# Optimization experiments

Measured on AMD Instinct MI355X. Metric: run time of the kernel, lower is better.

## Reference

```python
import jax, jax.numpy as jnp
import numpy as np

L = 48                 # lattice side
M = 2 * L * L          # 4608 spin-orbitals (spinful: 2 per site)
N_OCC = 1024           # occupied fermions
N_HID = 24             # hidden fermions
NT2 = 2 * N_HID        # pairing channels in CNN output
JASTROW = 16
CH = NT2 + JASTROW     # 64 CNN channels
NBLOCKS = 4
K = 3                  # conv kernel size


def conv2d_circular(x, w, b):
    # x: (C,H,W), w: (O,I,K,K); 'SAME' conv with circular (periodic) padding
    p = K // 2
    xp = jnp.pad(x, ((0, 0), (p, p), (p, p)), mode='wrap')
    y = jax.lax.conv_general_dilated(xp[None], w, (1, 1), 'VALID',
                                     dimension_numbers=('NCHW', 'OIHW', 'NCHW'))[0]
    if b is not None:
        y = y + b[:, None, None]
    return y


def cnn_forward(x, params):
    # ReshapeConv: flat spinful config (M,) -> (2, L, L)
    h = x.reshape(2, L, L)
    for i, (w1, b1, w2, b2) in enumerate(params):
        res = h
        t = h / jnp.sqrt(i + 1.0)
        t = t / jnp.sqrt(2.0) if i == 0 else jax.nn.gelu(t)
        t = jax.nn.gelu(conv2d_circular(t, w1, b1))
        t = conv2d_circular(t, w2, b2)
        if t.shape[0] > res.shape[0]:
            res = jnp.repeat(res, t.shape[0] // res.shape[0], axis=0)
        h = t + res
    return h / jnp.sqrt(NBLOCKS + 1.0)


def pfaffian_sign(A):
    # Sign of the Pfaffian of skew-symmetric A via Householder tridiagonalization.
    # pf(A) = det(Q) * prod(superdiag of T over even positions); det(Q)=(-1)^{#reflections}.
    n = A.shape[0]
    idx = jnp.arange(n)

    def body(k, carry):
        A, ds = carry
        col = A[:, k]
        xv = jnp.where(idx > k, col, 0.0)
        normx = jnp.sqrt(jnp.sum(xv * xv))
        s = jnp.where(col[k + 1] >= 0, 1.0, -1.0)
        v = xv - (-s * normx) * (idx == k + 1).astype(A.dtype)
        vn = jnp.sqrt(jnp.sum(v * v))
        ok = vn > 1e-30
        v = jnp.where(ok, v / jnp.where(ok, vn, 1.0), 0.0)
        u = A @ v
        # H A H for skew A with H = I - 2 v v^T  (v^T A v = 0)
        A = A + 2.0 * jnp.outer(v, u) - 2.0 * jnp.outer(u, v)
        return A, jnp.where(ok, -ds, ds)

    A, ds = jax.lax.fori_loop(0, n - 2, body, (A, jnp.array(1.0, A.dtype)))
    sup = jnp.diagonal(A, offset=1)[::2]
    return ds * jnp.prod(jnp.sign(sup))


def setup_inputs() -> dict:
    key = jax.random.key(0)
    ks = jax.random.split(key, 32)
    # occupation config in {+1,-1} with exactly N_OCC occupied modes
    occ = jnp.concatenate([jnp.ones(N_OCC, jnp.float32), -jnp.ones(M - N_OCC, jnp.float32)])
    x = jax.random.permutation(ks[0], occ)

    def he(k, shape):
        fan_in = shape[1] * shape[2] * shape[3]
        return jax.random.normal(k, shape, jnp.float32) * jnp.sqrt(2.0 / fan_in)

    inp = {
        'x': x,
        'F_vv': jax.random.normal(ks[1], (M, M), jnp.float32),
        'F_hh': jax.random.normal(ks[2], (N_HID, N_HID), jnp.float32),
    }
    j = 3
    for b in range(NBLOCKS):
        cin = 2 if b == 0 else CH
        inp[f'w1_{b}'] = he(ks[j], (CH, cin, K, K)); j += 1
        inp[f'b1_{b}'] = jnp.zeros((CH,), jnp.float32)
        inp[f'w2_{b}'] = he(ks[j], (CH, CH, K, K)); j += 1
        if b < NBLOCKS - 1:  # last block conv2 has no bias
            inp[f'b2_{b}'] = jnp.zeros((CH,), jnp.float32)
    return inp


def reference(x, F_vv, F_hh,
              w1_0, b1_0, w2_0, b2_0,
              w1_1, b1_1, w2_1, b2_1,
              w1_2, b1_2, w2_2, b2_2,
              w1_3, b1_3, w2_3):
    params = [(w1_0, b1_0, w2_0, b2_0),
              (w1_1, b1_1, w2_1, b2_1),
              (w1_2, b1_2, w2_2, b2_2),
              (w1_3, b1_3, w2_3, None)]
    out = cnn_forward(x, params)                     # (CH, L, L)
    n = jnp.nonzero(x == 1, size=N_OCC)[0]           # occupied mode indices
    log_J = out[NT2:].sum()                          # Jastrow log-factor (real)
    F_vh = out[:NT2].reshape(-1, M).T                # (M, N_HID)
    Fvv = 0.5 * (F_vv - F_vv.T)
    Fvh_n = F_vh[n]                                  # (N_OCC, N_HID)
    A = jnp.block([[Fvv[n][:, n], Fvh_n],
                   [-Fvh_n.T, 0.5 * (F_hh - F_hh.T)]])  # (N_OCC+N_HID,)^2 skew
    sign = pfaffian_sign(jax.lax.stop_gradient(A))   # cos(angle(sign)) == sign for real dtype
    logabspf = 0.5 * jnp.linalg.slogdet(A)[1]        # |pf(A)| = sqrt(|det(A)|)
    return sign, logabspf + log_J
```

## Files before the change

kernel.cpp:

```cpp
#include <hip/hip_runtime.h>
#include <math.h>


#define NPIX 2304
#define MSZ  4608
#define NOCC 1024
#define NHID 24
#define PF_N 1048

__device__ __forceinline__ float gelu_f(float v){
  float v3 = v*v*v;
  return 0.5f*v*(1.0f + tanhf(0.7978845608028654f*(v + 0.044715f*v3)));
}

__global__ void k_find_n(const float* __restrict__ x, int* __restrict__ nidx){
  __shared__ int cnt[256];
  __shared__ int off[256];
  int t = threadIdx.x;
  int c = 0;
  for (int k = 0; k < 18; k++) c += (x[t*18+k] == 1.0f) ? 1 : 0;
  cnt[t] = c;
  __syncthreads();
  if (t == 0){ int s = 0; for (int q=0;q<256;q++){ off[q]=s; s+=cnt[q]; } }
  __syncthreads();
  int o = off[t];
  for (int k = 0; k < 18; k++){
    int idx = t*18+k;
    if (x[idx] == 1.0f) nidx[o++] = idx;
  }
}

__global__ void k_pre(const float* __restrict__ in, float* __restrict__ outp,
                      int count, int dogelu, float scale){
  int g = blockIdx.x*256 + threadIdx.x;
  if (g >= count) return;
  float v = in[g]*scale;
  if (dogelu) v = gelu_f(v);
  outp[g] = v;
}

__global__ __launch_bounds__(256) void k_conv(const float* __restrict__ in,
      const float* __restrict__ wgt, const float* __restrict__ bias,
      const float* __restrict__ res, float* __restrict__ outp,
      int cin, int resmode, int dogelu, float scale){
  int c = blockIdx.x / 9;
  int p = (blockIdx.x % 9)*256 + threadIdx.x;
  int y = p / 48, x = p - y*48;
  int ym = ((y+47)%48)*48, y0 = y*48, yp = ((y+1)%48)*48;
  int xm = (x+47)%48, xq = (x+1)%48;
  float s = 0.f;
  const float* wp = wgt + c*cin*9;
  for (int ci = 0; ci < cin; ci++){
    const float* b_ = in + ci*NPIX;
    s += b_[ym+xm]*wp[0] + b_[ym+x]*wp[1] + b_[ym+xq]*wp[2]
       + b_[y0+xm]*wp[3] + b_[y0+x]*wp[4] + b_[y0+xq]*wp[5]
       + b_[yp+xm]*wp[6] + b_[yp+x]*wp[7] + b_[yp+xq]*wp[8];
    wp += 9;
  }
  if (bias) s += bias[c];
  if (dogelu) s = gelu_f(s);
  if (resmode == 1) s += res[c*NPIX + p];
  else if (resmode == 2) s += res[(c>>5)*NPIX + p];
  s *= scale;
  outp[c*NPIX + p] = s;
}

__global__ void k_logJ(const float* __restrict__ hfin, double* __restrict__ acc){
  int g = blockIdx.x*256 + threadIdx.x;
  double v = (double)hfin[48*NPIX + g];
  for (int o = 32; o > 0; o >>= 1) v += __shfl_down(v, o, 64);
  __shared__ double wsum[4];
  int lane = threadIdx.x & 63, wv = threadIdx.x >> 6;
  if (lane == 0) wsum[wv] = v;
  __syncthreads();
  if (threadIdx.x == 0) atomicAdd(acc, wsum[0]+wsum[1]+wsum[2]+wsum[3]);
}

__device__ __forceinline__ double fvh_val(const float* h, int m, int r){
  int s = (m >= NPIX) ? 1 : 0;
  int p = m - s*NPIX;
  return (double)h[(2*r+s)*NPIX + p];
}

__global__ void k_buildA(const float* __restrict__ Fvv, const float* __restrict__ Fhh,
                         const float* __restrict__ hfin, const int* __restrict__ nidx,
                         double* __restrict__ A){
  int g = blockIdx.x*256 + threadIdx.x;
  if (g >= PF_N*PF_N) return;
  int i = g / PF_N, j = g - i*PF_N;
  if (j >= i) return;
  double v;
  if (i < NOCC){
    int ni = nidx[i], nj = nidx[j];
    v = 0.5*((double)Fvv[(size_t)ni*MSZ + nj] - (double)Fvv[(size_t)nj*MSZ + ni]);
  } else if (j < NOCC){
    v = -fvh_val(hfin, nidx[j], i - NOCC);
  } else {
    int r = i - NOCC, r2 = j - NOCC;
    v = 0.5*((double)Fhh[r*NHID + r2] - (double)Fhh[r2*NHID + r]);
  }
  A[(size_t)i*PF_N + j] = v;
}

__device__ __forceinline__ void factor_lds(double* D, double* sTf, int w,
      double* __restrict__ histN, double* __restrict__ lacc,
      int* __restrict__ nneg){
  const int tid = threadIdx.x;
  const int r = tid & 63, qu = tid >> 6;
  const int np = w >> 1;
  for (int j = 0; j < np; j++){
    const int r0 = 2*j, r1 = r0 + 1;
    const double t = -D[r1*65 + r0];
    const double invt = 1.0 / t;
    if (tid == 0) sTf[j] = t;
    const bool rowok = (r < w) && (r >= r0 + 2);
    if (rowok){
      const double ar = D[r*65 + r0], br = D[r*65 + r1];
      if (qu == 0){
        histN[32 + j*64 + r]        = ar * invt;
        histN[32 + 2048 + j*64 + r] = br * invt;
      }
      const int lo = r0 + 2, hi = r;
      const int per = (hi - lo + 3) >> 2;
      const int cb = lo + qu*per;
      int ce = cb + per; if (ce > hi) ce = hi;
      for (int c = cb; c < ce; c++){
        const double ac = D[c*65 + r0], bc = D[c*65 + r1];
        D[r*65 + c] += (br*ac - ar*bc) * invt;
      }
    }
    __syncthreads();
  }
  if (tid < np) histN[tid] = 1.0 / sTf[tid];
  if (tid < 64){
    double lv = 0.0; int sg = 0;
    if (tid < np){ double t = sTf[tid]; lv = log(fabs(t)); sg = (t < 0.0) ? 1 : 0; }
    for (int o = 32; o > 0; o >>= 1){
      lv += __shfl_down(lv, o, 64);
      sg += __shfl_down(sg, o, 64);
    }
    if (tid == 0){ atomicAdd(lacc, lv); atomicAdd(nneg, sg); }
  }
}

__global__ __launch_bounds__(256) void k_panelD0(const double* __restrict__ A,
      double* __restrict__ hist, double* __restrict__ lacc,
      int* __restrict__ nneg){
  __shared__ double D[64*65];
  __shared__ double sTf[32];
  const int tid = threadIdx.x;
  for (int idx = tid; idx < 64*64; idx += 256){
    int r = idx >> 6, c = idx & 63;
    if (r > c) D[r*65+c] = A[(size_t)r*PF_N + c];
  }
  __syncthreads();
  factor_lds(D, sTf, 64, hist, lacc, nneg);
}

__global__ __launch_bounds__(256) void k_panelR(double* __restrict__ A,
      const double* __restrict__ hist, int k){
  const int N = PF_N, c0 = 64*k, tc0 = c0 + 64;
  const int wv = threadIdx.x >> 6, lc = threadIdx.x & 63;
  const int i = tc0 + blockIdx.x*4 + wv;
  if (i >= N) return;
  double v = A[(size_t)i*N + c0 + lc];
  const double* hA = hist + 32;
  const double* hB = hist + 32 + 2048;
  #pragma unroll 8
  for (int j = 0; j < 32; j++){
    double a = __shfl(v, 2*j,   64);
    double b = __shfl(v, 2*j+1, 64);
    if (lc >= 2*j+2) v += b*hA[j*64+lc] - a*hB[j*64+lc];
  }
  A[(size_t)i*N + c0 + lc] = v;
}

__global__ __launch_bounds__(256) void k_trail(double* __restrict__ A,
      const double* __restrict__ histR, double* __restrict__ histW,
      double* __restrict__ lacc, int* __restrict__ nneg, int k){
  const int N = PF_N, c0 = 64*k, tc0 = c0 + 64;
  const int tid = threadIdx.x;
  int I = 0, item = blockIdx.x;
  while ((I+1)*(I+2)/2 <= item) I++;
  const int J = item - I*(I+1)/2;
  const int i0 = tc0 + I*64, j0 = tc0 + J*64;
  const int iend = (i0 + 64 < N) ? (i0 + 64) : N;
  const int jend = (j0 + 64 < N) ? (j0 + 64) : N;
  __shared__ double shmem[4224];
  __shared__ double sInvL[32];
  __shared__ double sTf[32];
  double* sPiA = shmem;
  double* sPiB = shmem + 1056;
  double* sPjA = shmem + 2112;
  double* sPjB = shmem + 3168;
  if (tid < 32) sInvL[tid] = histR[tid];
  const int ty = tid >> 4, tx = tid & 15;
  double acc[4][4];
  #pragma unroll
  for (int rr = 0; rr < 4; rr++)
    #pragma unroll
    for (int cc = 0; cc < 4; cc++){
      const int i = i0 + ty + 16*rr, j = j0 + tx + 16*cc;
      acc[rr][cc] = (i < iend && j < jend && i > j) ? A[(size_t)i*N + j] : 0.0;
    }
  __syncthreads();
  #pragma unroll
  for (int lh = 0; lh < 2; lh++){
    #pragma unroll
    for (int u = 0; u < 4; u++){
      const int idx = tid + u*256;
      const int r = idx >> 4, ll = idx & 15;
      const int l = lh*16 + ll;
      const double it = sInvL[l];
      const int gi = i0 + r;
      double a = 0.0, b = 0.0;
      if (gi < iend){
        a = A[(size_t)gi*N + c0 + 2*l];
        b = A[(size_t)gi*N + c0 + 2*l + 1];
      }
      sPiA[ll*66+r] = a; sPiB[ll*66+r] = b;
      const int gj = j0 + r;
      double a2 = 0.0, b2 = 0.0;
      if (gj < jend){
        a2 = A[(size_t)gj*N + c0 + 2*l];
        b2 = A[(size_t)gj*N + c0 + 2*l + 1];
      }
      sPjA[ll*66+r] = a2*it; sPjB[ll*66+r] = b2*it;
    }
    __syncthreads();
    #pragma unroll 4
    for (int ll = 0; ll < 16; ll++){
      double ar[4], br[4], ac[4], bc[4];
      #pragma unroll
      for (int rr = 0; rr < 4; rr++){
        ar[rr] = sPiA[ll*66 + ty + 16*rr];
        br[rr] = sPiB[ll*66 + ty + 16*rr];
      }
      #pragma unroll
      for (int cc = 0; cc < 4; cc++){
        ac[cc] = sPjA[ll*66 + tx + 16*cc];
        bc[cc] = sPjB[ll*66 + tx + 16*cc];
      }
      #pragma unroll
      for (int rr = 0; rr < 4; rr++)
        #pragma unroll
        for (int cc = 0; cc < 4; cc++)
          acc[rr][cc] += br[rr]*ac[cc] - ar[rr]*bc[cc];
    }
    __syncthreads();
  }
  #pragma unroll
  for (int rr = 0; rr < 4; rr++)
    #pragma unroll
    for (int cc = 0; cc < 4; cc++){
      const int i = i0 + ty + 16*rr, j = j0 + tx + 16*cc;
      if (i < iend && j < jend && i > j) A[(size_t)i*N + j] = acc[rr][cc];
    }
  if (blockIdx.x == 0){
    __syncthreads();
    const int wn = iend - i0;
    #pragma unroll
    for (int rr = 0; rr < 4; rr++)
      #pragma unroll
      for (int cc = 0; cc < 4; cc++){
        const int i = i0 + ty + 16*rr, j = j0 + tx + 16*cc;
        if (i < iend && j < jend && i > j)
          shmem[(i - i0)*65 + (j - j0)] = acc[rr][cc];
      }
    __syncthreads();
    factor_lds(shmem, sTf, wn, histW, lacc, nneg);
  }
}

__global__ void k_out(const double* __restrict__ lacc, const int* __restrict__ nneg,
                      const double* __restrict__ logJ, float* __restrict__ outp){
  if (threadIdx.x == 0){
    outp[0] = (*nneg & 1) ? -1.0f : 1.0f;
    outp[1] = (float)(*lacc + *logJ);
  }
}

extern "C" void kernel_launch(void* const* d_in, const int* in_sizes, int n_in,
                              void* d_out, int out_size, void* d_ws, size_t ws_size,
                              hipStream_t stream){
  (void)in_sizes; (void)n_in; (void)out_size; (void)ws_size;
  const float* x   = (const float*)d_in[0];
  const float* Fvv = (const float*)d_in[1];
  const float* Fhh = (const float*)d_in[2];
  const float* w1[4] = {(const float*)d_in[3], (const float*)d_in[7],
                        (const float*)d_in[11], (const float*)d_in[15]};
  const float* b1[4] = {(const float*)d_in[4], (const float*)d_in[8],
                        (const float*)d_in[12], (const float*)d_in[16]};
  const float* w2[4] = {(const float*)d_in[5], (const float*)d_in[9],
                        (const float*)d_in[13], (const float*)d_in[17]};
  const float* b2[3] = {(const float*)d_in[6], (const float*)d_in[10],
                        (const float*)d_in[14]};

  char* ws = (char*)d_ws;
  double* lacc  = (double*)(ws + 0);
  int*    nneg  = (int*)(ws + 8);
  double* logJa = (double*)(ws + 1024);
  int*    nidx  = (int*)(ws + 1088);
  double* hist0 = (double*)(ws + 8192);
  double* hist1 = (double*)(ws + 41216);
  const size_t CB = 589824;
  float* tbuf  = (float*)(ws + 74240);
  float* ybuf  = (float*)(ws + 74240 + CB);
  float* hbuf0 = (float*)(ws + 74240 + 2*CB);
  float* hbuf1 = (float*)(ws + 74240 + 3*CB);
  double* A    = (double*)(ws + 74240 + 4*CB);

  hipMemsetAsync(d_ws, 0, 2048, stream);
  k_find_n<<<1,256,0,stream>>>(x, nidx);

  k_pre <<<18, 256,0,stream>>>(x, tbuf, 4608, 0, 0.70710678118654752f);
  k_conv<<<576,256,0,stream>>>(tbuf, w1[0], b1[0], nullptr, ybuf, 2, 0, 1, 1.0f);
  k_conv<<<576,256,0,stream>>>(ybuf, w2[0], b2[0], x,      hbuf0, 64, 2, 0, 1.0f);
  k_pre <<<576,256,0,stream>>>(hbuf0, tbuf, 147456, 1, 0.70710678118654752f);
  k_conv<<<576,256,0,stream>>>(tbuf, w1[1], b1[1], nullptr, ybuf, 64, 0, 1, 1.0f);
  k_conv<<<576,256,0,stream>>>(ybuf, w2[1], b2[1], hbuf0,  hbuf1, 64, 1, 0, 1.0f);
  k_pre <<<576,256,0,stream>>>(hbuf1, tbuf, 147456, 1, 0.57735026918962576f);
  k_conv<<<576,256,0,stream>>>(tbuf, w1[2], b1[2], nullptr, ybuf, 64, 0, 1, 1.0f);
  k_conv<<<576,256,0,stream>>>(ybuf, w2[2], b2[2], hbuf1,  hbuf0, 64, 1, 0, 1.0f);
  k_pre <<<576,256,0,stream>>>(hbuf0, tbuf, 147456, 1, 0.5f);
  k_conv<<<576,256,0,stream>>>(tbuf, w1[3], b1[3], nullptr, ybuf, 64, 0, 1, 1.0f);
  k_conv<<<576,256,0,stream>>>(ybuf, w2[3], nullptr, hbuf0, hbuf1, 64, 1, 0,
                               0.44721359549995794f);

  k_logJ  <<<144,256,0,stream>>>(hbuf1, logJa);
  k_buildA<<<(PF_N*PF_N+255)/256,256,0,stream>>>(Fvv, Fhh, hbuf1, nidx, A);

  k_panelD0<<<1,256,0,stream>>>(A, hist0, lacc, nneg);
  for (int k = 0; k < 16; k++){
    double* hR = (k & 1) ? hist1 : hist0;
    double* hW = (k & 1) ? hist0 : hist1;
    const int m = PF_N - 64*(k+1);
    k_panelR<<<(m+3)/4,256,0,stream>>>(A, hR, k);
    const int nt = (m + 63) >> 6;
    k_trail<<<nt*(nt+1)/2,256,0,stream>>>(A, hR, hW, lacc, nneg, k);
  }
  k_out<<<1,64,0,stream>>>(lacc, nneg, logJa, (float*)d_out);
}
```

Baseline: 1.128 ms.

## Fuse CNN pre-activation and logJ into conv, tile Fvv gather, fold output into trail

The pre-activation (scale+gelu) pass is folded into the conv epilogue, and the x scaling is moved into the index-finding kernel. The Jastrow sum is reduced inside the last conv. Each conv thread now computes three horizontally adjacent outputs so neighbouring input loads are reused. The Fvv gather for A is done in 32x32 shared-memory tiles over the lower triangle only, so the transposed read is coalesced. The final output write is moved into the last trailing-update kernel, which removes the separate output launch. This cuts launches and memory traffic at the cost of a more complex conv epilogue, and correctness of the final output now depends on the atomic return values and on that block finishing last.

```diff
diff --git a/kernel.cpp b/kernel.cpp
--- a/kernel.cpp
+++ b/kernel.cpp
@@ -13,12 +13,18 @@
   return 0.5f*v*(1.0f + tanhf(0.7978845608028654f*(v + 0.044715f*v3)));
 }
 
-__global__ void k_find_n(const float* __restrict__ x, int* __restrict__ nidx){
+__global__ void k_prep(const float* __restrict__ x, int* __restrict__ nidx,
+                       float* __restrict__ tbuf){
   __shared__ int cnt[256];
   __shared__ int off[256];
   int t = threadIdx.x;
   int c = 0;
-  for (int k = 0; k < 18; k++) c += (x[t*18+k] == 1.0f) ? 1 : 0;
+  for (int k = 0; k < 18; k++){
+    int idx = t*18 + k;
+    float v = x[idx];
+    c += (v == 1.0f) ? 1 : 0;
+    tbuf[idx] = v * 0.70710678118654752f;
+  }
   cnt[t] = c;
   __syncthreads();
   if (t == 0){ int s = 0; for (int q=0;q<256;q++){ off[q]=s; s+=cnt[q]; } }
@@ -30,81 +36,108 @@
   }
 }
 
-__global__ void k_pre(const float* __restrict__ in, float* __restrict__ outp,
-                      int count, int dogelu, float scale){
-  int g = blockIdx.x*256 + threadIdx.x;
-  if (g >= count) return;
-  float v = in[g]*scale;
-  if (dogelu) v = gelu_f(v);
-  outp[g] = v;
-}
-
-__global__ __launch_bounds__(256) void k_conv(const float* __restrict__ in,
+__global__ __launch_bounds__(128) void k_conv(const float* __restrict__ in,
       const float* __restrict__ wgt, const float* __restrict__ bias,
       const float* __restrict__ res, float* __restrict__ outp,
-      int cin, int resmode, int dogelu, float scale){
-  int c = blockIdx.x / 9;
-  int p = (blockIdx.x % 9)*256 + threadIdx.x;
-  int y = p / 48, x = p - y*48;
-  int ym = ((y+47)%48)*48, y0 = y*48, yp = ((y+1)%48)*48;
-  int xm = (x+47)%48, xq = (x+1)%48;
-  float s = 0.f;
+      float* __restrict__ pre_out, double* __restrict__ logJ_acc,
+      int cin, int resmode, int dogelu, float scale, float pre_scale){
+  const int c  = blockIdx.x / 6;
+  const int rg = blockIdx.x % 6;
+  const int tid = threadIdx.x;
+  const int y  = rg*8 + (tid >> 4);
+  const int xg = (tid & 15)*3;
+  const int ym = ((y+47)%48)*48, y0 = y*48, yp = ((y+1)%48)*48;
+  int c5[5];
+  #pragma unroll
+  for (int t = 0; t < 5; t++){
+    int xx = xg - 1 + t;
+    c5[t] = (xx < 0) ? 47 : ((xx >= 48) ? xx - 48 : xx);
+  }
+  float s0 = 0.f, s1 = 0.f, s2 = 0.f;
   const float* wp = wgt + c*cin*9;
   for (int ci = 0; ci < cin; ci++){
     const float* b_ = in + ci*NPIX;
-    s += b_[ym+xm]*wp[0] + b_[ym+x]*wp[1] + b_[ym+xq]*wp[2]
-       + b_[y0+xm]*wp[3] + b_[y0+x]*wp[4] + b_[y0+xq]*wp[5]
-       + b_[yp+xm]*wp[6] + b_[yp+x]*wp[7] + b_[yp+xq]*wp[8];
+    #pragma unroll
+    for (int rr = 0; rr < 3; rr++){
+      const int rb = (rr == 0) ? ym : ((rr == 1) ? y0 : yp);
+      float v0 = b_[rb+c5[0]], v1 = b_[rb+c5[1]], v2 = b_[rb+c5[2]];
+      float v3 = b_[rb+c5[3]], v4 = b_[rb+c5[4]];
+      float w0 = wp[3*rr], w1 = wp[3*rr+1], w2 = wp[3*rr+2];
+      s0 += v0*w0 + v1*w1 + v2*w2;
+      s1 += v1*w0 + v2*w1 + v3*w2;
+      s2 += v2*w0 + v3*w1 + v4*w2;
+    }
     wp += 9;
   }
-  if (bias) s += bias[c];
-  if (dogelu) s = gelu_f(s);
-  if (resmode == 1) s += res[c*NPIX + p];
-  else if (resmode == 2) s += res[(c>>5)*NPIX + p];
-  s *= scale;
-  outp[c*NPIX + p] = s;
-}
-
-__global__ void k_logJ(const float* __restrict__ hfin, double* __restrict__ acc){
+  const float bv = bias ? bias[c] : 0.f;
+  const int base = c*NPIX + y0 + xg;
+  float sv[3] = {s0, s1, s2};
+  double ls = 0.0;
+  #pragma unroll
+  for (int t = 0; t < 3; t++){
+    float s = sv[t] + bv;
+    if (dogelu) s = gelu_f(s);
+    if (resmode == 1) s += res[c*NPIX + y0 + xg + t];
+    else if (resmode == 2) s += res[(c>>5)*NPIX + y0 + xg + t];
+    s *= scale;
+    outp[base+t] = s;
+    if (pre_out) pre_out[base+t] = gelu_f(s * pre_scale);
+    ls += (double)s;
+  }
+  if (logJ_acc && c >= 48){
+    for (int o = 32; o > 0; o >>= 1) ls += __shfl_down(ls, o, 64);
+    if ((tid & 63) == 0) atomicAdd(logJ_acc, ls);
+  }
+}
+
+__global__ __launch_bounds__(256) void k_buildAvv(const float* __restrict__ Fvv,
+      const int* __restrict__ nidx, double* __restrict__ A){
+  __shared__ float G1[32][33], G2[32][33];
+  __shared__ int sNi[32], sNj[32];
+  int I = 0, item = blockIdx.x;
+  while ((I+1)*(I+2)/2 <= item) I++;
+  const int J = item - I*(I+1)/2;
+  const int i0 = I*32, j0 = J*32;
+  const int tid = threadIdx.x;
+  if (tid < 32){ sNi[tid] = nidx[i0+tid]; }
+  else if (tid < 64){ sNj[tid-32] = nidx[j0+tid-32]; }
+  __syncthreads();
+  for (int idx = tid; idx < 32*32; idx += 256){
+    const int r = idx >> 5, c = idx & 31;
+    G1[r][c] = Fvv[(size_t)sNi[r]*MSZ + sNj[c]];
+    G2[r][c] = Fvv[(size_t)sNj[r]*MSZ + sNi[c]];
+  }
+  __syncthreads();
+  for (int idx = tid; idx < 32*32; idx += 256){
+    const int r = idx >> 5, c = idx & 31;
+    const int i = i0 + r, j = j0 + c;
+    if (i > j)
+      A[(size_t)i*PF_N + j] = 0.5*((double)G1[r][c] - (double)G2[c][r]);
+  }
+}
+
+__global__ void k_buildAs(const float* __restrict__ Fhh,
+      const float* __restrict__ hfin, const int* __restrict__ nidx,
+      double* __restrict__ A){
   int g = blockIdx.x*256 + threadIdx.x;
-  double v = (double)hfin[48*NPIX + g];
-  for (int o = 32; o > 0; o >>= 1) v += __shfl_down(v, o, 64);
-  __shared__ double wsum[4];
-  int lane = threadIdx.x & 63, wv = threadIdx.x >> 6;
-  if (lane == 0) wsum[wv] = v;
-  __syncthreads();
-  if (threadIdx.x == 0) atomicAdd(acc, wsum[0]+wsum[1]+wsum[2]+wsum[3]);
-}
-
-__device__ __forceinline__ double fvh_val(const float* h, int m, int r){
-  int s = (m >= NPIX) ? 1 : 0;
-  int p = m - s*NPIX;
-  return (double)h[(2*r+s)*NPIX + p];
-}
-
-__global__ void k_buildA(const float* __restrict__ Fvv, const float* __restrict__ Fhh,
-                         const float* __restrict__ hfin, const int* __restrict__ nidx,
-                         double* __restrict__ A){
-  int g = blockIdx.x*256 + threadIdx.x;
-  if (g >= PF_N*PF_N) return;
-  int i = g / PF_N, j = g - i*PF_N;
+  if (g >= 24*PF_N) return;
+  const int i = NOCC + g / PF_N, j = g % PF_N;
   if (j >= i) return;
+  const int r = i - NOCC;
   double v;
-  if (i < NOCC){
-    int ni = nidx[i], nj = nidx[j];
-    v = 0.5*((double)Fvv[(size_t)ni*MSZ + nj] - (double)Fvv[(size_t)nj*MSZ + ni]);
-  } else if (j < NOCC){
-    v = -fvh_val(hfin, nidx[j], i - NOCC);
+  if (j < NOCC){
+    int nj = nidx[j];
+    int ss = (nj >= NPIX) ? 1 : 0;
+    v = -(double)hfin[(2*r+ss)*NPIX + (nj - ss*NPIX)];
   } else {
-    int r = i - NOCC, r2 = j - NOCC;
+    int r2 = j - NOCC;
     v = 0.5*((double)Fhh[r*NHID + r2] - (double)Fhh[r2*NHID + r]);
   }
   A[(size_t)i*PF_N + j] = v;
 }
 
 __device__ __forceinline__ void factor_lds(double* D, double* sTf, int w,
-      double* __restrict__ histN, double* __restrict__ lacc,
-      int* __restrict__ nneg){
+      double* __restrict__ histN, double& lv_out, int& sg_out){
   const int tid = threadIdx.x;
   const int r = tid & 63, qu = tid >> 6;
   const int np = w >> 1;
@@ -132,6 +165,7 @@
     __syncthreads();
   }
   if (tid < np) histN[tid] = 1.0 / sTf[tid];
+  lv_out = 0.0; sg_out = 0;
   if (tid < 64){
     double lv = 0.0; int sg = 0;
     if (tid < np){ double t = sTf[tid]; lv = log(fabs(t)); sg = (t < 0.0) ? 1 : 0; }
@@ -139,7 +173,7 @@
       lv += __shfl_down(lv, o, 64);
       sg += __shfl_down(sg, o, 64);
     }
-    if (tid == 0){ atomicAdd(lacc, lv); atomicAdd(nneg, sg); }
+    if (tid == 0){ lv_out = lv; sg_out = sg; }
   }
 }
 
@@ -154,7 +188,9 @@
     if (r > c) D[r*65+c] = A[(size_t)r*PF_N + c];
   }
   __syncthreads();
-  factor_lds(D, sTf, 64, hist, lacc, nneg);
+  double lv; int sg;
+  factor_lds(D, sTf, 64, hist, lv, sg);
+  if (tid == 0){ atomicAdd(lacc, lv); atomicAdd(nneg, sg); }
 }
 
 __global__ __launch_bounds__(256) void k_panelR(double* __restrict__ A,
@@ -177,7 +213,9 @@
 
 __global__ __launch_bounds__(256) void k_trail(double* __restrict__ A,
       const double* __restrict__ histR, double* __restrict__ histW,
-      double* __restrict__ lacc, int* __restrict__ nneg, int k){
+      double* __restrict__ lacc, int* __restrict__ nneg,
+      const double* __restrict__ logJ, float* __restrict__ outp,
+      int k, int fin){
   const int N = PF_N, c0 = 64*k, tc0 = c0 + 64;
   const int tid = threadIdx.x;
   int I = 0, item = blockIdx.x;
@@ -268,15 +306,17 @@
           shmem[(i - i0)*65 + (j - j0)] = acc[rr][cc];
       }
     __syncthreads();
-    factor_lds(shmem, sTf, wn, histW, lacc, nneg);
-  }
-}
-
-__global__ void k_out(const double* __restrict__ lacc, const int* __restrict__ nneg,
-                      const double* __restrict__ logJ, float* __restrict__ outp){
-  if (threadIdx.x == 0){
-    outp[0] = (*nneg & 1) ? -1.0f : 1.0f;
-    outp[1] = (float)(*lacc + *logJ);
+    double lv; int sg;
+    factor_lds(shmem, sTf, wn, histW, lv, sg);
+    if (tid == 0){
+      double lold = atomicAdd(lacc, lv);
+      int sold = atomicAdd(nneg, sg);
+      if (fin){
+        int stot = sold + sg;
+        outp[0] = (stot & 1) ? -1.0f : 1.0f;
+        outp[1] = (float)(lold + lv + logJ[0]);
+      }
+    }
   }
 }
 
@@ -311,24 +351,30 @@
   double* A    = (double*)(ws + 74240 + 4*CB);
 
   hipMemsetAsync(d_ws, 0, 2048, stream);
-  k_find_n<<<1,256,0,stream>>>(x, nidx);
-
-  k_pre <<<18, 256,0,stream>>>(x, tbuf, 4608, 0, 0.70710678118654752f);
-  k_conv<<<576,256,0,stream>>>(tbuf, w1[0], b1[0], nullptr, ybuf, 2, 0, 1, 1.0f);
-  k_conv<<<576,256,0,stream>>>(ybuf, w2[0], b2[0], x,      hbuf0, 64, 2, 0, 1.0f);
-  k_pre <<<576,256,0,stream>>>(hbuf0, tbuf, 147456, 1, 0.70710678118654752f);
-  k_conv<<<576,256,0,stream>>>(tbuf, w1[1], b1[1], nullptr, ybuf, 64, 0, 1, 1.0f);
-  k_conv<<<576,256,0,stream>>>(ybuf, w2[1], b2[1], hbuf0,  hbuf1, 64, 1, 0, 1.0f);
-  k_pre <<<576,256,0,stream>>>(hbuf1, tbuf, 147456, 1, 0.57735026918962576f);
-  k_conv<<<576,256,0,stream>>>(tbuf, w1[2], b1[2], nullptr, ybuf, 64, 0, 1, 1.0f);
-  k_conv<<<576,256,0,stream>>>(ybuf, w2[2], b2[2], hbuf1,  hbuf0, 64, 1, 0, 1.0f);
-  k_pre <<<576,256,0,stream>>>(hbuf0, tbuf, 147456, 1, 0.5f);
-  k_conv<<<576,256,0,stream>>>(tbuf, w1[3], b1[3], nullptr, ybuf, 64, 0, 1, 1.0f);
-  k_conv<<<576,256,0,stream>>>(ybuf, w2[3], nullptr, hbuf0, hbuf1, 64, 1, 0,
-                               0.44721359549995794f);
-
-  k_logJ  <<<144,256,0,stream>>>(hbuf1, logJa);
-  k_buildA<<<(PF_N*PF_N+255)/256,256,0,stream>>>(Fvv, Fhh, hbuf1, nidx, A);
+  k_prep<<<1,256,0,stream>>>(x, nidx, tbuf);
+
+  k_conv<<<384,128,0,stream>>>(tbuf, w1[0], b1[0], nullptr, ybuf,
+                               nullptr, nullptr, 2, 0, 1, 1.0f, 0.f);
+  k_conv<<<384,128,0,stream>>>(ybuf, w2[0], b2[0], x, hbuf0,
+                               tbuf, nullptr, 64, 2, 0, 1.0f,
+                               0.70710678118654752f);
+  k_conv<<<384,128,0,stream>>>(tbuf, w1[1], b1[1], nullptr, ybuf,
+                               nullptr, nullptr, 64, 0, 1, 1.0f, 0.f);
+  k_conv<<<384,128,0,stream>>>(ybuf, w2[1], b2[1], hbuf0, hbuf1,
+                               tbuf, nullptr, 64, 1, 0, 1.0f,
+                               0.57735026918962576f);
+  k_conv<<<384,128,0,stream>>>(tbuf, w1[2], b1[2], nullptr, ybuf,
+                               nullptr, nullptr, 64, 0, 1, 1.0f, 0.f);
+  k_conv<<<384,128,0,stream>>>(ybuf, w2[2], b2[2], hbuf1, hbuf0,
+                               tbuf, nullptr, 64, 1, 0, 1.0f, 0.5f);
+  k_conv<<<384,128,0,stream>>>(tbuf, w1[3], b1[3], nullptr, ybuf,
+                               nullptr, nullptr, 64, 0, 1, 1.0f, 0.f);
+  k_conv<<<384,128,0,stream>>>(ybuf, w2[3], nullptr, hbuf0, hbuf1,
+                               nullptr, logJa, 64, 1, 0,
+                               0.44721359549995794f, 0.f);
+
+  k_buildAvv<<<528,256,0,stream>>>(Fvv, nidx, A);
+  k_buildAs<<<(24*PF_N+255)/256,256,0,stream>>>(Fhh, hbuf1, nidx, A);
 
   k_panelD0<<<1,256,0,stream>>>(A, hist0, lacc, nneg);
   for (int k = 0; k < 16; k++){
@@ -337,7 +383,7 @@
     const int m = PF_N - 64*(k+1);
     k_panelR<<<(m+3)/4,256,0,stream>>>(A, hR, k);
     const int nt = (m + 63) >> 6;
-    k_trail<<<nt*(nt+1)/2,256,0,stream>>>(A, hR, hW, lacc, nneg, k);
-  }
-  k_out<<<1,64,0,stream>>>(lacc, nneg, logJa, (float*)d_out);
-}
+    k_trail<<<nt*(nt+1)/2,256,0,stream>>>(A, hR, hW, lacc, nneg, logJa,
+                                          (float*)d_out, k, (k == 15) ? 1 : 0);
+  }
+}
```

Result: no change. 1.121 ms (-0.7%).
